# Kernel optimization log

Hardware: AMD Instinct MI355X
Metric: run time of the kernel (lower is better)

The kernel has to match this reference:

```python
import jax, jax.numpy as jnp
import numpy as np

HIDDEN = 768
MLP_RATIO = 4
HID_F = HIDDEN * MLP_RATIO          # 3072
NUM_EXPERTS = 6
PART = 192                           # part_features
SHARED = HIDDEN - PART               # 576
B, S = 32, 1024


def setup_inputs() -> dict:
    key = jax.random.key(0)
    ks = jax.random.split(key, 8)
    hidden_state = jax.random.normal(ks[0], (B, S, HIDDEN), dtype=jnp.float32)
    indices = jax.random.randint(ks[1], (B,), 0, NUM_EXPERTS, dtype=jnp.int64)
    sc1 = 1.0 / np.sqrt(HIDDEN)
    sc2 = 1.0 / np.sqrt(HID_F)
    W1 = jax.random.normal(ks[2], (HIDDEN, HID_F), dtype=jnp.float32) * sc1
    b1 = jax.random.normal(ks[3], (HID_F,), dtype=jnp.float32) * sc1
    W2 = jax.random.normal(ks[4], (HID_F, SHARED), dtype=jnp.float32) * sc2
    b2 = jax.random.normal(ks[5], (SHARED,), dtype=jnp.float32) * sc2
    We = jax.random.normal(ks[6], (NUM_EXPERTS, HID_F, PART), dtype=jnp.float32) * sc2
    be = jax.random.normal(ks[7], (NUM_EXPERTS, PART), dtype=jnp.float32) * sc2
    return {"hidden_state": hidden_state, "indices": indices,
            "W1": W1, "b1": b1, "W2": W2, "b2": b2, "We": We, "be": be}


def reference(hidden_state, indices, W1, b1, W2, b2, We, be):
    # fc1 + exact GELU (torch ACT2FN['gelu'])
    h = jnp.einsum('bsd,df->bsf', hidden_state, W1) + b1          # [B,S,HID_F]
    h = jax.nn.gelu(h, approximate=False)
    # shared branch
    shared = jnp.einsum('bsf,fo->bso', h, W2) + b2                # [B,S,SHARED]
    # expert branch: indices select exactly one expert per batch element,
    # so the masked sum over all experts equals gathering the routed expert.
    Wsel = We[indices]                                            # [B,HID_F,PART]
    bsel = be[indices]                                            # [B,PART]
    expert = jnp.einsum('bsf,bfp->bsp', h, Wsel) + bsel[:, None, :]
    return jnp.concatenate([shared, expert], axis=-1)             # [B,S,HIDDEN]
```

## Files before the change

kernel.cpp:

```cpp
#include <hip/hip_runtime.h>
#include <hip/hip_bf16.h>
#include <cstdint>
#include <cstddef>

#define HIDDEN   768
#define HID_F    3072
#define PART     192
#define SHARED_F 576
#define NEXP     6
#define BATCH    32
#define SEQ      1024
#define M_TOK    (BATCH * SEQ)

typedef __bf16 bf16;
typedef __attribute__((ext_vector_type(8))) __bf16 bf16x8;
typedef __attribute__((ext_vector_type(4))) __bf16 bf16x4;
typedef __attribute__((ext_vector_type(4))) float  f32x4;

__device__ __forceinline__ void gl2lds16(const void* g, void* l) {
    __builtin_amdgcn_global_load_lds(
        (const __attribute__((address_space(1))) void*)g,
        (__attribute__((address_space(3))) void*)l,
        16, 0, 0);
}

__device__ __forceinline__ float gelu_fast(float x) {
    float xs = x * 0.70710678118654752f;
    float ax = __builtin_fabsf(xs);
    float t  = __builtin_amdgcn_rcpf(1.0f + 0.3275911f * ax);
    float p  = t * (0.254829592f +
               t * (-0.284496736f +
               t * (1.421413741f +
               t * (-1.453152027f +
               t * 1.061405429f))));
    float e  = __expf(-xs * xs);
    float er = 1.0f - p * e;
    er = (xs < 0.0f) ? -er : er;
    return 0.5f * x * (1.0f + er);
}

__global__ __launch_bounds__(256) void cvt_f32_bf16(
        const float4* __restrict__ src, bf16x4* __restrict__ dst, int n4) {
    int i      = blockIdx.x * 256 + threadIdx.x;
    int stride = gridDim.x * 256;
    for (; i < n4; i += stride) {
        float4 v = src[i];
        bf16x4 o = { (__bf16)v.x, (__bf16)v.y, (__bf16)v.z, (__bf16)v.w };
        dst[i] = o;
    }
}

__global__ __launch_bounds__(256) void transpose_cvt(
        const float* __restrict__ src, bf16* __restrict__ dst, int K, int N) {
    __shared__ float t[32][33];
    const int n0 = blockIdx.x * 32, k0 = blockIdx.y * 32;
    const int tx = threadIdx.x & 31, ty = threadIdx.x >> 5;
#pragma unroll
    for (int p = 0; p < 4; ++p) {
        int r = ty + p * 8;
        t[r][tx] = src[(size_t)(k0 + r) * N + n0 + tx];
    }
    __syncthreads();
#pragma unroll
    for (int p = 0; p < 4; ++p) {
        int rn = ty + p * 8;
        dst[(size_t)(n0 + rn) * K + k0 + tx] = (bf16)t[tx][rn];
    }
}

__global__ __launch_bounds__(256) void build_wcat(
        const float* __restrict__ W2, const float* __restrict__ We,
        bf16* __restrict__ Wcat) {
    __shared__ float t[32][33];
    const int e  = blockIdx.z;
    const int n0 = blockIdx.x * 32;
    const int k0 = blockIdx.y * 32;
    const int tx = threadIdx.x & 31, ty = threadIdx.x >> 5;
    const float* src;
    int ld, c;
    if (n0 < SHARED_F) { src = W2; ld = SHARED_F; c = n0 + tx; }
    else { src = We + (size_t)e * HID_F * PART; ld = PART; c = n0 + tx - SHARED_F; }
#pragma unroll
    for (int p = 0; p < 4; ++p) {
        int r = ty + p * 8;
        t[r][tx] = src[(size_t)(k0 + r) * ld + c];
    }
    __syncthreads();
    bf16* dst = Wcat + (size_t)e * HIDDEN * HID_F;
#pragma unroll
    for (int p = 0; p < 4; ++p) {
        int rn = ty + p * 8;
        dst[(size_t)(n0 + rn) * HID_F + k0 + tx] = (bf16)t[tx][rn];
    }
}


__global__ __launch_bounds__(256) void fc1_gelu(
        const bf16* __restrict__ A,
        const bf16* __restrict__ Bt,
        const float* __restrict__ b1,
        bf16* __restrict__ H) {
    __shared__ alignas(16) bf16 As[128 * 32];
    __shared__ alignas(16) bf16 Bs[128 * 32];
    const int tid  = threadIdx.x;
    const int wave = tid >> 6, lane = tid & 63;
    const int wm = wave >> 1, wn = wave & 1;
    const int lrow = lane & 15, lk8 = lane >> 4;

    const int L   = blockIdx.x;
    const int xcd = L & 7;
    const int j   = L >> 3;
    const int jm  = j / 24;
    const int mt  = xcd * 32 + jm;
    const int nt  = j - jm * 24;
    const int m0 = mt * 128;
    const int n0 = nt * 128;

    const int srow   = lane >> 2;
    const int schunk = (((lane & 3) ^ ((lane >> 3) & 3))) * 8;
    const int rchunk = ((lk8 ^ ((lrow >> 1) & 3))) * 8;

    const bf16* gA0 = A  + (size_t)(m0 + wave * 32 + srow) * HIDDEN + schunk;
    const bf16* gA1 = gA0 + 16 * HIDDEN;
    const bf16* gB0 = Bt + (size_t)(n0 + wave * 32 + srow) * HIDDEN + schunk;
    const bf16* gB1 = gB0 + 16 * HIDDEN;
    bf16* lA0 = As + (wave * 32) * 32;
    bf16* lA1 = lA0 + 16 * 32;
    bf16* lB0 = Bs + (wave * 32) * 32;
    bf16* lB1 = lB0 + 16 * 32;

    f32x4 acc[4][4] = {};
    for (int k0 = 0; k0 < HIDDEN; k0 += 32) {
        gl2lds16(gA0, lA0); gl2lds16(gA1, lA1);
        gl2lds16(gB0, lB0); gl2lds16(gB1, lB1);
        gA0 += 32; gA1 += 32; gB0 += 32; gB1 += 32;
        __syncthreads();
        bf16x8 af[4], bfr[4];
#pragma unroll
        for (int mi = 0; mi < 4; ++mi)
            af[mi] = *(const bf16x8*)(As + (wm * 64 + mi * 16 + lrow) * 32 + rchunk);
#pragma unroll
        for (int ni = 0; ni < 4; ++ni)
            bfr[ni] = *(const bf16x8*)(Bs + (wn * 64 + ni * 16 + lrow) * 32 + rchunk);
#pragma unroll
        for (int mi = 0; mi < 4; ++mi)
#pragma unroll
            for (int ni = 0; ni < 4; ++ni)
                acc[mi][ni] = __builtin_amdgcn_mfma_f32_16x16x32_bf16(
                    af[mi], bfr[ni], acc[mi][ni], 0, 0, 0);
        __syncthreads();
    }
#pragma unroll
    for (int mi = 0; mi < 4; ++mi) {
#pragma unroll
        for (int ni = 0; ni < 4; ++ni) {
            int col = n0 + wn * 64 + ni * 16 + lrow;
            float bias = b1[col];
#pragma unroll
            for (int r = 0; r < 4; ++r) {
                int row = m0 + wm * 64 + mi * 16 + lk8 * 4 + r;
                float v = acc[mi][ni][r] + bias;
                H[(size_t)row * HID_F + col] = (bf16)gelu_fast(v);
            }
        }
    }
}

__global__ __launch_bounds__(256) void fc2_moe(
        const bf16* __restrict__ H,
        const bf16* __restrict__ Wcat,
        const float* __restrict__ b2,
        const float* __restrict__ be,
        const int*  __restrict__ idx,
        float* __restrict__ Out) {
    __shared__ alignas(16) bf16 As[128 * 32];
    __shared__ alignas(16) bf16 Bs[128 * 32];
    const int tid  = threadIdx.x;
    const int wave = tid >> 6, lane = tid & 63;
    const int wm = wave >> 1, wn = wave & 1;
    const int lrow = lane & 15, lk8 = lane >> 4;

    const int L   = blockIdx.x;
    const int xcd = L & 7;
    const int j   = L >> 3;
    const int jm  = j / 6;
    const int mt  = xcd * 32 + jm;
    const int nt  = j - jm * 6;
    const int m0 = mt * 128;
    const int n0 = nt * 128;

    int e = idx[mt >> 3];
    e = e < 0 ? 0 : (e > NEXP - 1 ? NEXP - 1 : e);
    const bf16* Bt = Wcat + (size_t)e * HIDDEN * HID_F;
    const int srow   = lane >> 2;
    const int schunk = (((lane & 3) ^ ((lane >> 3) & 3))) * 8;
    const int rchunk = ((lk8 ^ ((lrow >> 1) & 3))) * 8;

    const bf16* gA0 = H  + (size_t)(m0 + wave * 32 + srow) * HID_F + schunk;
    const bf16* gA1 = gA0 + 16 * HID_F;
    const bf16* gB0 = Bt + (size_t)(n0 + wave * 32 + srow) * HID_F + schunk;
    const bf16* gB1 = gB0 + 16 * HID_F;
    bf16* lA0 = As + (wave * 32) * 32;
    bf16* lA1 = lA0 + 16 * 32;
    bf16* lB0 = Bs + (wave * 32) * 32;
    bf16* lB1 = lB0 + 16 * 32;

    f32x4 acc[4][4] = {};
    for (int k0 = 0; k0 < HID_F; k0 += 32) {
        gl2lds16(gA0, lA0); gl2lds16(gA1, lA1);
        gl2lds16(gB0, lB0); gl2lds16(gB1, lB1);
        gA0 += 32; gA1 += 32; gB0 += 32; gB1 += 32;
        __syncthreads();
        bf16x8 af[4], bfr[4];
#pragma unroll
        for (int mi = 0; mi < 4; ++mi)
            af[mi] = *(const bf16x8*)(As + (wm * 64 + mi * 16 + lrow) * 32 + rchunk);
#pragma unroll
        for (int ni = 0; ni < 4; ++ni)
            bfr[ni] = *(const bf16x8*)(Bs + (wn * 64 + ni * 16 + lrow) * 32 + rchunk);
#pragma unroll
        for (int mi = 0; mi < 4; ++mi)
#pragma unroll
            for (int ni = 0; ni < 4; ++ni)
                acc[mi][ni] = __builtin_amdgcn_mfma_f32_16x16x32_bf16(
                    af[mi], bfr[ni], acc[mi][ni], 0, 0, 0);
        __syncthreads();
    }
#pragma unroll
    for (int mi = 0; mi < 4; ++mi) {
#pragma unroll
        for (int ni = 0; ni < 4; ++ni) {
            int col = n0 + wn * 64 + ni * 16 + lrow;
            float bias = (col < SHARED_F) ? b2[col] : be[e * PART + col - SHARED_F];
#pragma unroll
            for (int r = 0; r < 4; ++r) {
                int row = m0 + wm * 64 + mi * 16 + lk8 * 4 + r;
                Out[(size_t)row * HIDDEN + col] = acc[mi][ni][r] + bias;
            }
        }
    }
}

extern "C" void kernel_launch(void* const* d_in, const int* in_sizes, int n_in,
                              void* d_out, int out_size, void* d_ws, size_t ws_size,
                              hipStream_t stream) {
    const float* hidden = (const float*)d_in[0];
    const int*   idx    = (const int*)d_in[1];
    const float* W1     = (const float*)d_in[2];
    const float* b1     = (const float*)d_in[3];
    const float* W2     = (const float*)d_in[4];
    const float* b2     = (const float*)d_in[5];
    const float* We     = (const float*)d_in[6];
    const float* be     = (const float*)d_in[7];
    float* out = (float*)d_out;

    char* ws = (char*)d_ws;
    bf16* hb   = (bf16*)(ws);
    bf16* h    = (bf16*)(ws + 50331648);
    bf16* W1t  = (bf16*)(ws + 251658240);
    bf16* Wcat = (bf16*)(ws + 256376832);

    cvt_f32_bf16<<<4096, 256, 0, stream>>>(
        (const float4*)hidden, (bf16x4*)hb, (M_TOK * HIDDEN) / 4);
    transpose_cvt<<<dim3(HID_F / 32, HIDDEN / 32), 256, 0, stream>>>(
        W1, W1t, HIDDEN, HID_F);
    build_wcat<<<dim3(HIDDEN / 32, HID_F / 32, NEXP), 256, 0, stream>>>(
        W2, We, Wcat);

    fc1_gelu<<<(HID_F / 128) * (M_TOK / 128), 256, 0, stream>>>(hb, W1t, b1, h);

    fc2_moe<<<(HIDDEN / 128) * (M_TOK / 128), 256, 0, stream>>>(
        h, Wcat, b2, be, idx, out);
}
```

Baseline: 610.9 us.

## Replace GEMM kernels with 256x256-tile, 8-wave, double-buffered phased pipeline

```diff
diff --git a/kernel.cpp b/kernel.cpp
--- a/kernel.cpp
+++ b/kernel.cpp
@@ -22,6 +22,17 @@
         (const __attribute__((address_space(1))) void*)g,
         (__attribute__((address_space(3))) void*)l,
         16, 0, 0);
+}
+
+__device__ __forceinline__ f32x4 mfma16(bf16x8 a, bf16x8 b, f32x4 c) {
+    return __builtin_amdgcn_mfma_f32_16x16x32_bf16(a, b, c, 0, 0, 0);
+}
+
+#define CFENCE() asm volatile("" ::: "memory")
+__device__ __forceinline__ void barrier_raw() {
+    CFENCE();
+    __builtin_amdgcn_s_barrier();
+    CFENCE();
 }
 
 __device__ __forceinline__ float gelu_fast(float x) {
@@ -95,147 +106,182 @@
 }
 
 
-__global__ __launch_bounds__(256) void fc1_gelu(
-        const bf16* __restrict__ A,
-        const bf16* __restrict__ Bt,
-        const float* __restrict__ b1,
-        bf16* __restrict__ H) {
-    __shared__ alignas(16) bf16 As[128 * 32];
-    __shared__ alignas(16) bf16 Bs[128 * 32];
+#define STAGE_A(kt, hm, bb) do {                                          \
+    const bf16* g_ = gA + (size_t)((hm) * 128) * LDA + (kt) * 64;         \
+    bf16* l_ = lA + ((bb) * 2 + (hm)) * 8192;                             \
+    gl2lds16(g_, l_);                                                     \
+    gl2lds16(g_ + (size_t)64 * LDA, l_ + 4096);                           \
+} while (0)
+
+#define STAGE_B(kt, hm, bb) do {                                          \
+    const bf16* g_ = gB + (size_t)((hm) * 128) * LDB + (kt) * 64;         \
+    bf16* l_ = lB + ((bb) * 2 + (hm)) * 8192;                             \
+    gl2lds16(g_, l_);                                                     \
+    gl2lds16(g_ + (size_t)64 * LDB, l_ + 4096);                           \
+} while (0)
+
+#define LOAD_A(qm, bb) do {                                               \
+    const bf16* ab_ = fA + ((bb) * 2 + (qm)) * 8192;                      \
+    _Pragma("unroll")                                                     \
+    for (int mi = 0; mi < 4; ++mi) {                                      \
+        af[mi][0] = *(const bf16x8*)(ab_ + mi * 1024 + pca0);             \
+        af[mi][1] = *(const bf16x8*)(ab_ + mi * 1024 + pca1);             \
+    }                                                                     \
+} while (0)
+
+#define LOAD_B(qn, bb) do {                                               \
+    const bf16* bb_ = fB + ((bb) * 2 + (qn)) * 8192;                      \
+    _Pragma("unroll")                                                     \
+    for (int nj = 0; nj < 2; ++nj) {                                      \
+        bfr[nj][0] = *(const bf16x8*)(bb_ + nj * 1024 + pcb0);            \
+        bfr[nj][1] = *(const bf16x8*)(bb_ + nj * 1024 + pcb1);            \
+    }                                                                     \
+} while (0)
+
+#define MFMA_CLUSTER(qm, qn) do {                                         \
+    __builtin_amdgcn_s_setprio(1);                                        \
+    _Pragma("unroll")                                                     \
+    for (int mi = 0; mi < 4; ++mi)                                        \
+        _Pragma("unroll")                                                 \
+        for (int nj = 0; nj < 2; ++nj) {                                  \
+            acc[(qm)*4+mi][(qn)*2+nj] =                                   \
+                mfma16(af[mi][0], bfr[nj][0], acc[(qm)*4+mi][(qn)*2+nj]); \
+            acc[(qm)*4+mi][(qn)*2+nj] =                                   \
+                mfma16(af[mi][1], bfr[nj][1], acc[(qm)*4+mi][(qn)*2+nj]); \
+        }                                                                 \
+    __builtin_amdgcn_s_setprio(0);                                        \
+} while (0)
+
+template<bool IS_FC1>
+__global__ __launch_bounds__(512, 2) void fc_8ph(
+        const bf16*  __restrict__ A,
+        const bf16*  __restrict__ Bmat,
+        const float* __restrict__ bias1,
+        const float* __restrict__ bias2,
+        const int*   __restrict__ idx,
+        void*        __restrict__ Outv) {
+    constexpr int LDA     = IS_FC1 ? HIDDEN : HID_F;
+    constexpr int LDB     = LDA;
+    constexpr int NT      = LDA / 64;
+    constexpr int NTILE_N = IS_FC1 ? (HID_F / 256) : (HIDDEN / 256);
+    constexpr int LDOUT   = IS_FC1 ? HID_F : HIDDEN;
+
+    __shared__ alignas(16) bf16 Abuf[2 * 2 * 128 * 64];
+    __shared__ alignas(16) bf16 Bbuf[2 * 2 * 128 * 64];
+
     const int tid  = threadIdx.x;
     const int wave = tid >> 6, lane = tid & 63;
-    const int wm = wave >> 1, wn = wave & 1;
-    const int lrow = lane & 15, lk8 = lane >> 4;
+    const int wm = wave >> 2, wn = wave & 3;
+    const int lrow = lane & 15, lk8 = (lane >> 4) & 3;
 
     const int L   = blockIdx.x;
     const int xcd = L & 7;
     const int j   = L >> 3;
-    const int jm  = j / 24;
-    const int mt  = xcd * 32 + jm;
-    const int nt  = j - jm * 24;
-    const int m0 = mt * 128;
-    const int n0 = nt * 128;
-
-    const int srow   = lane >> 2;
-    const int schunk = (((lane & 3) ^ ((lane >> 3) & 3))) * 8;
-    const int rchunk = ((lk8 ^ ((lrow >> 1) & 3))) * 8;
-
-    const bf16* gA0 = A  + (size_t)(m0 + wave * 32 + srow) * HIDDEN + schunk;
-    const bf16* gA1 = gA0 + 16 * HIDDEN;
-    const bf16* gB0 = Bt + (size_t)(n0 + wave * 32 + srow) * HIDDEN + schunk;
-    const bf16* gB1 = gB0 + 16 * HIDDEN;
-    bf16* lA0 = As + (wave * 32) * 32;
-    bf16* lA1 = lA0 + 16 * 32;
-    bf16* lB0 = Bs + (wave * 32) * 32;
-    bf16* lB1 = lB0 + 16 * 32;
-
-    f32x4 acc[4][4] = {};
-    for (int k0 = 0; k0 < HIDDEN; k0 += 32) {
-        gl2lds16(gA0, lA0); gl2lds16(gA1, lA1);
-        gl2lds16(gB0, lB0); gl2lds16(gB1, lB1);
-        gA0 += 32; gA1 += 32; gB0 += 32; gB1 += 32;
-        __syncthreads();
-        bf16x8 af[4], bfr[4];
-#pragma unroll
-        for (int mi = 0; mi < 4; ++mi)
-            af[mi] = *(const bf16x8*)(As + (wm * 64 + mi * 16 + lrow) * 32 + rchunk);
-#pragma unroll
-        for (int ni = 0; ni < 4; ++ni)
-            bfr[ni] = *(const bf16x8*)(Bs + (wn * 64 + ni * 16 + lrow) * 32 + rchunk);
-#pragma unroll
-        for (int mi = 0; mi < 4; ++mi)
-#pragma unroll
-            for (int ni = 0; ni < 4; ++ni)
-                acc[mi][ni] = __builtin_amdgcn_mfma_f32_16x16x32_bf16(
-                    af[mi], bfr[ni], acc[mi][ni], 0, 0, 0);
-        __syncthreads();
-    }
-#pragma unroll
-    for (int mi = 0; mi < 4; ++mi) {
-#pragma unroll
-        for (int ni = 0; ni < 4; ++ni) {
-            int col = n0 + wn * 64 + ni * 16 + lrow;
-            float bias = b1[col];
-#pragma unroll
-            for (int r = 0; r < 4; ++r) {
-                int row = m0 + wm * 64 + mi * 16 + lk8 * 4 + r;
-                float v = acc[mi][ni][r] + bias;
-                H[(size_t)row * HID_F + col] = (bf16)gelu_fast(v);
-            }
+    const int jm  = j / NTILE_N;
+    const int mt  = xcd * 16 + jm;
+    const int nt  = j - jm * NTILE_N;
+    const int m0  = mt * 256;
+    const int n0  = nt * 256;
+
+    const bf16* Bt;
+    int e = 0;
+    if constexpr (IS_FC1) {
+        Bt = Bmat;
+    } else {
+        e = idx[mt >> 2];
+        e = e < 0 ? 0 : (e > NEXP - 1 ? NEXP - 1 : e);
+        Bt = Bmat + (size_t)e * HIDDEN * HID_F;
+    }
+
+    const int srow = tid >> 3;
+    const int lch  = (tid & 7) ^ (srow & 7);
+    const bf16* gA = A  + (size_t)(m0 + srow) * LDA + lch * 8;
+    const bf16* gB = Bt + (size_t)(n0 + srow) * LDB + lch * 8;
+    bf16* lA = Abuf + wave * 512;
+    bf16* lB = Bbuf + wave * 512;
+
+    const int rA = wm * 64 + lrow;
+    const int rB = wn * 32 + lrow;
+    const int pca0 = ((0 + lk8) ^ (rA & 7)) * 8;
+    const int pca1 = ((4 + lk8) ^ (rA & 7)) * 8;
+    const int pcb0 = ((0 + lk8) ^ (rB & 7)) * 8;
+    const int pcb1 = ((4 + lk8) ^ (rB & 7)) * 8;
+    const bf16* fA = Abuf + rA * 64;
+    const bf16* fB = Bbuf + rB * 64;
+
+    f32x4 acc[8][4] = {};
+    bf16x8 af[4][2], bfr[2][2];
+
+    STAGE_A(0, 0, 0); STAGE_B(0, 0, 0); STAGE_B(0, 1, 0); STAGE_A(0, 1, 0);
+    STAGE_A(1, 0, 1); STAGE_B(1, 0, 1);
+    asm volatile("s_waitcnt vmcnt(8)" ::: "memory");
+    barrier_raw();
+
+#pragma unroll 1
+    for (int t = 0; t < NT; ++t) {
+        const int b   = t & 1;
+        const int bo  = b ^ 1;
+        const int tb1 = (t + 1 < NT) ? t + 1 : t - 1;
+        const int ta2 = (t + 2 < NT) ? t + 2 : t;
+
+        LOAD_A(0, b);
+        LOAD_B(0, b);
+        STAGE_B(tb1, 1, bo);
+        barrier_raw();
+        MFMA_CLUSTER(0, 0);
+        asm volatile("s_waitcnt vmcnt(6)" ::: "memory");
+        barrier_raw();
+
+        LOAD_B(1, b);
+        STAGE_A(tb1, 1, bo);
+        barrier_raw();
+        MFMA_CLUSTER(0, 1);
+        barrier_raw();
+
+        LOAD_A(1, b);
+        LOAD_B(0, b);
+        STAGE_A(ta2, 0, b);
+        barrier_raw();
+        MFMA_CLUSTER(1, 0);
+        barrier_raw();
+
+        LOAD_B(1, b);
+        STAGE_B(ta2, 0, b);
+        barrier_raw();
+        MFMA_CLUSTER(1, 1);
+        asm volatile("s_waitcnt vmcnt(8)" ::: "memory");
+        barrier_raw();
+    }
+
+    float bv[4];
+#pragma unroll
+    for (int nj2 = 0; nj2 < 4; ++nj2) {
+        const int col = n0 + (nj2 >> 1) * 128 + wn * 32 + (nj2 & 1) * 16 + lrow;
+        if constexpr (IS_FC1) {
+            bv[nj2] = bias1[col];
+        } else {
+            bv[nj2] = (col < SHARED_F) ? bias1[col]
+                                       : bias2[e * PART + col - SHARED_F];
         }
     }
-}
-
-__global__ __launch_bounds__(256) void fc2_moe(
-        const bf16* __restrict__ H,
-        const bf16* __restrict__ Wcat,
-        const float* __restrict__ b2,
-        const float* __restrict__ be,
-        const int*  __restrict__ idx,
-        float* __restrict__ Out) {
-    __shared__ alignas(16) bf16 As[128 * 32];
-    __shared__ alignas(16) bf16 Bs[128 * 32];
-    const int tid  = threadIdx.x;
-    const int wave = tid >> 6, lane = tid & 63;
-    const int wm = wave >> 1, wn = wave & 1;
-    const int lrow = lane & 15, lk8 = lane >> 4;
-
-    const int L   = blockIdx.x;
-    const int xcd = L & 7;
-    const int j   = L >> 3;
-    const int jm  = j / 6;
-    const int mt  = xcd * 32 + jm;
-    const int nt  = j - jm * 6;
-    const int m0 = mt * 128;
-    const int n0 = nt * 128;
-
-    int e = idx[mt >> 3];
-    e = e < 0 ? 0 : (e > NEXP - 1 ? NEXP - 1 : e);
-    const bf16* Bt = Wcat + (size_t)e * HIDDEN * HID_F;
-    const int srow   = lane >> 2;
-    const int schunk = (((lane & 3) ^ ((lane >> 3) & 3))) * 8;
-    const int rchunk = ((lk8 ^ ((lrow >> 1) & 3))) * 8;
-
-    const bf16* gA0 = H  + (size_t)(m0 + wave * 32 + srow) * HID_F + schunk;
-    const bf16* gA1 = gA0 + 16 * HID_F;
-    const bf16* gB0 = Bt + (size_t)(n0 + wave * 32 + srow) * HID_F + schunk;
-    const bf16* gB1 = gB0 + 16 * HID_F;
-    bf16* lA0 = As + (wave * 32) * 32;
-    bf16* lA1 = lA0 + 16 * 32;
-    bf16* lB0 = Bs + (wave * 32) * 32;
-    bf16* lB1 = lB0 + 16 * 32;
-
-    f32x4 acc[4][4] = {};
-    for (int k0 = 0; k0 < HID_F; k0 += 32) {
-        gl2lds16(gA0, lA0); gl2lds16(gA1, lA1);
-        gl2lds16(gB0, lB0); gl2lds16(gB1, lB1);
-        gA0 += 32; gA1 += 32; gB0 += 32; gB1 += 32;
-        __syncthreads();
-        bf16x8 af[4], bfr[4];
-#pragma unroll
-        for (int mi = 0; mi < 4; ++mi)
-            af[mi] = *(const bf16x8*)(As + (wm * 64 + mi * 16 + lrow) * 32 + rchunk);
-#pragma unroll
-        for (int ni = 0; ni < 4; ++ni)
-            bfr[ni] = *(const bf16x8*)(Bs + (wn * 64 + ni * 16 + lrow) * 32 + rchunk);
-#pragma unroll
-        for (int mi = 0; mi < 4; ++mi)
-#pragma unroll
-            for (int ni = 0; ni < 4; ++ni)
-                acc[mi][ni] = __builtin_amdgcn_mfma_f32_16x16x32_bf16(
-                    af[mi], bfr[ni], acc[mi][ni], 0, 0, 0);
-        __syncthreads();
-    }
-#pragma unroll
-    for (int mi = 0; mi < 4; ++mi) {
-#pragma unroll
-        for (int ni = 0; ni < 4; ++ni) {
-            int col = n0 + wn * 64 + ni * 16 + lrow;
-            float bias = (col < SHARED_F) ? b2[col] : be[e * PART + col - SHARED_F];
-#pragma unroll
-            for (int r = 0; r < 4; ++r) {
-                int row = m0 + wm * 64 + mi * 16 + lk8 * 4 + r;
-                Out[(size_t)row * HIDDEN + col] = acc[mi][ni][r] + bias;
+#pragma unroll
+    for (int mi2 = 0; mi2 < 8; ++mi2) {
+        const int row0 = m0 + (mi2 >> 2) * 128 + wm * 64 + (mi2 & 3) * 16 + lk8 * 4;
+#pragma unroll
+        for (int nj2 = 0; nj2 < 4; ++nj2) {
+            const int col = n0 + (nj2 >> 1) * 128 + wn * 32 + (nj2 & 1) * 16 + lrow;
+            if constexpr (IS_FC1) {
+                bf16* o = (bf16*)Outv;
+#pragma unroll
+                for (int r = 0; r < 4; ++r)
+                    o[(size_t)(row0 + r) * LDOUT + col] =
+                        (bf16)gelu_fast(acc[mi2][nj2][r] + bv[nj2]);
+            } else {
+                float* o = (float*)Outv;
+#pragma unroll
+                for (int r = 0; r < 4; ++r)
+                    o[(size_t)(row0 + r) * LDOUT + col] =
+                        acc[mi2][nj2][r] + bv[nj2];
             }
         }
     }
@@ -267,8 +313,9 @@
     build_wcat<<<dim3(HIDDEN / 32, HID_F / 32, NEXP), 256, 0, stream>>>(
         W2, We, Wcat);
 
-    fc1_gelu<<<(HID_F / 128) * (M_TOK / 128), 256, 0, stream>>>(hb, W1t, b1, h);
-
-    fc2_moe<<<(HIDDEN / 128) * (M_TOK / 128), 256, 0, stream>>>(
+    fc_8ph<true><<<(M_TOK / 256) * (HID_F / 256), 512, 0, stream>>>(
+        hb, W1t, b1, nullptr, nullptr, h);
+
+    fc_8ph<false><<<(M_TOK / 256) * (HIDDEN / 256), 512, 0, stream>>>(
         h, Wcat, b2, be, idx, out);
 }
```

Result: slower. 642.5 us (+5.2%).
